# Kernel optimization log

Hardware: AMD Instinct MI355X
Metric: run time of the kernel (lower is better)

Reference implementation:

```python
import jax, jax.numpy as jnp
import numpy as np

DIM = 256
GRID = 5


def setup_inputs() -> dict:
    key = jax.random.key(0)
    kx, kw = jax.random.split(key)
    x = jax.random.normal(kx, (32, 2048, DIM), dtype=jnp.float32)
    scale = 1.0 / (np.sqrt(DIM) * np.sqrt(GRID))
    fourier_weight = jax.random.normal(kw, (2, DIM, DIM, GRID), dtype=jnp.float32) * scale
    bias = jnp.zeros((DIM,), dtype=jnp.float32)
    return {"x": x, "fourier_weight": fourier_weight, "bias": bias}


def reference(x, fourier_weight, bias):
    D = bias.shape[0]
    G = fourier_weight.shape[-1]
    out_shape = x.shape[:-1] + (D,)
    xf = x.reshape(-1, D)                                  # (N, D)
    k = jnp.arange(1, G + 1, dtype=x.dtype)                # (G,)
    arg = xf[:, :, None] * k                               # (N, D, G)
    # y[n,o] = sum_{d,g} cos(k_g x[n,d]) W[0,o,d,g] + sin(k_g x[n,d]) W[1,o,d,g] + b[o]
    y = jnp.einsum('ndg,odg->no', jnp.cos(arg), fourier_weight[0])
    y = y + jnp.einsum('ndg,odg->no', jnp.sin(arg), fourier_weight[1])
    y = y + bias
    return y.reshape(out_shape)
```

## Files before the change

kernel.cpp:

```cpp
#include <hip/hip_runtime.h>
#include <hip/hip_bf16.h>
#include <stdint.h>

#define DIM 256
#define GRID_G 5
#define KTOT (DIM * GRID_G * 2)
#define BM 256
#define BN 256
#define BK 64
#define NTHREADS 512
#define NCHUNK (KTOT / BK)
#define AS_SH (BM * BK)
#define BS_SH (BN * BK)

typedef float f32x4 __attribute__((ext_vector_type(4)));
typedef short bf16x8 __attribute__((ext_vector_type(8)));

static __device__ __forceinline__ uint32_t f2bf_bits(float v) {
    uint32_t u = __float_as_uint(v);
    return (u + 0x7FFFu + ((u >> 16) & 1u)) >> 16;
}

static __device__ __forceinline__ void gload_lds16(const void* g, void* l) {
    __builtin_amdgcn_global_load_lds(
        (const __attribute__((address_space(1))) void*)g,
        (__attribute__((address_space(3))) void*)l, 16, 0, 0);
}

__global__ void wtransform(const float* __restrict__ W, uint16_t* __restrict__ Wb) {
    int idx = blockIdx.x * blockDim.x + threadIdx.x;
    if (idx >= DIM * KTOT) return;
    int o = idx / KTOT;
    int k = idx - o * KTOT;
    int g = k >> 9;
    int r = k & 511;
    int d = r >> 1;
    int s = r & 1;
    float w = W[(((s * DIM + o) * DIM + d) * GRID_G) + g];
    Wb[idx] = (uint16_t)f2bf_bits(w);
}

__global__ __launch_bounds__(NTHREADS, 2)
void fourier_gemm(const float* __restrict__ x, const uint16_t* __restrict__ Wb,
                  const float* __restrict__ bias, float* __restrict__ out) {
    __shared__ __align__(16) short As[2 * AS_SH];
    __shared__ __align__(16) short Bs[2 * BS_SH];

    const int tid  = threadIdx.x;
    const int lane = tid & 63;
    const int wave = tid >> 6;
    const int wrow = wave >> 2;
    const int wcol = wave & 3;
    const int row0 = blockIdx.x * BM;
    const int q16  = (lane >> 4) << 4;

    f32x4 acc[8][4];
#pragma unroll
    for (int m = 0; m < 8; ++m)
#pragma unroll
        for (int n = 0; n < 4; ++n)
            acc[m][n] = (f32x4){0.f, 0.f, 0.f, 0.f};

    const int sd2 = tid & 15;
    const int sn  = tid >> 4;

    float2 xq[8];

#define STAGE_B(cc, buf)                                                      \
    {                                                                         \
        const char* wbb = (const char*)Wb + (size_t)(cc) * 128;               \
        char* dst = (char*)(Bs + (buf) * BS_SH);                              \
        _Pragma("unroll")                                                     \
        for (int i = 0; i < 4; ++i) {                                         \
            int f = tid * 16 + i * 8192;                                      \
            int o = f >> 7;                                                   \
            int col = f & 127;                                                \
            int scol = col ^ ((o & 7) << 4);                                  \
            gload_lds16(wbb + (size_t)o * (KTOT * 2) + scol, dst + f);        \
        }                                                                     \
    }

#define LOAD_X(cc)                                                            \
    {                                                                         \
        int d0 = ((cc) & 7) * 32;                                             \
        _Pragma("unroll")                                                     \
        for (int i = 0; i < 8; ++i) {                                         \
            int n = sn + i * 32;                                              \
            xq[i] = *(const float2*)&x[(size_t)(row0 + n) * DIM + d0 + 2 * sd2]; \
        }                                                                     \
    }

#define TRIG_WRITE(cc, buf)                                                   \
    {                                                                         \
        float kgrev = (float)(((cc) >> 3) + 1) * 0.15915494309189535f;        \
        char* abase = (char*)(As + (buf) * AS_SH);                            \
        _Pragma("unroll")                                                     \
        for (int i = 0; i < 8; ++i) {                                         \
            int n = sn + i * 32;                                              \
            float r0 = xq[i].x * kgrev;                                       \
            float r1 = xq[i].y * kgrev;                                       \
            float s0, c0, s1, c1;                                             \
            asm("v_sin_f32 %0, %1" : "=v"(s0) : "v"(r0));                     \
            asm("v_cos_f32 %0, %1" : "=v"(c0) : "v"(r0));                     \
            asm("v_sin_f32 %0, %1" : "=v"(s1) : "v"(r1));                     \
            asm("v_cos_f32 %0, %1" : "=v"(c1) : "v"(r1));                     \
            uint32_t p0, p1;                                                  \
            asm("v_cvt_pk_bf16_f32 %0, %1, %2" : "=v"(p0) : "v"(c0), "v"(s0));\
            asm("v_cvt_pk_bf16_f32 %0, %1, %2" : "=v"(p1) : "v"(c1), "v"(s1));\
            int boff = (n * 128 + sd2 * 8) ^ ((n & 7) << 4);                  \
            uint64_t pk = ((uint64_t)p1 << 32) | (uint64_t)p0;                \
            *(uint64_t*)(abase + boff) = pk;                                  \
        }                                                                     \
    }

    STAGE_B(0, 0);
    LOAD_X(0);
    TRIG_WRITE(0, 0);
    __syncthreads();

    for (int c = 0; c < NCHUNK; ++c) {
        const int cur = c & 1;
        const int nxt = cur ^ 1;

        if (c + 1 < NCHUNK) {
            STAGE_B(c + 1, nxt);
            LOAD_X(c + 1);
        }

        const char* Ac = (const char*)(As + cur * AS_SH);
        const char* Bc = (const char*)(Bs + cur * BS_SH);

#pragma unroll
        for (int ks = 0; ks < 2; ++ks) {
            bf16x8 af[8], bfr[4];
#pragma unroll
            for (int m = 0; m < 8; ++m) {
                int r = wrow * 128 + m * 16 + (lane & 15);
                int off = (r * 128 + ks * 64 + q16) ^ ((r & 7) << 4);
                af[m] = *(const bf16x8*)(Ac + off);
            }
#pragma unroll
            for (int nf = 0; nf < 4; ++nf) {
                int o = wcol * 64 + nf * 16 + (lane & 15);
                int off = (o * 128 + ks * 64 + q16) ^ ((o & 7) << 4);
                bfr[nf] = *(const bf16x8*)(Bc + off);
            }
#pragma unroll
            for (int m = 0; m < 8; ++m)
#pragma unroll
                for (int nf = 0; nf < 4; ++nf)
                    acc[m][nf] = __builtin_amdgcn_mfma_f32_16x16x32_bf16(
                        af[m], bfr[nf], acc[m][nf], 0, 0, 0);
        }

        if (c + 1 < NCHUNK) {
            TRIG_WRITE(c + 1, nxt);
        }

        __syncthreads();
    }

#pragma unroll
    for (int nf = 0; nf < 4; ++nf) {
        int ocol = wcol * 64 + nf * 16 + (lane & 15);
        float b = bias[ocol];
#pragma unroll
        for (int m = 0; m < 8; ++m) {
            int rbase = row0 + wrow * 128 + m * 16 + ((lane >> 4) << 2);
#pragma unroll
            for (int r = 0; r < 4; ++r) {
                out[(size_t)(rbase + r) * DIM + ocol] = acc[m][nf][r] + b;
            }
        }
    }
}

extern "C" void kernel_launch(void* const* d_in, const int* in_sizes, int n_in,
                              void* d_out, int out_size, void* d_ws, size_t ws_size,
                              hipStream_t stream) {
    const float* x    = (const float*)d_in[0];
    const float* W    = (const float*)d_in[1];
    const float* bias = (const float*)d_in[2];
    float* out        = (float*)d_out;
    uint16_t* Wb      = (uint16_t*)d_ws;

    int rows = in_sizes[0] / DIM;
    int wtot = DIM * KTOT;

    hipLaunchKernelGGL(wtransform, dim3((wtot + 255) / 256), dim3(256), 0, stream, W, Wb);
    hipLaunchKernelGGL(fourier_gemm, dim3(rows / BM), dim3(NTHREADS), 0, stream,
                       x, Wb, bias, out);
}
```

Baseline: 200.5 us.

## Read B fragments directly from global, halve row tile, reorder K loop to reuse x loads

The GEMM kernel stops staging the bf16 weight matrix through LDS and instead has each wave load its B fragments straight from global memory (expected to hit L2). The row tile drops from 256 to 128, LDS use shrinks to the A buffer only, and occupancy is raised to 4 blocks per CU. The K loop is reordered so each slice of x is loaded once and reused across all five frequency multiples, which removes four of every five x reloads. The weight-transform kernel now writes 16-byte vectors per thread. The risk is higher global and L2 traffic for the weights with less latency hiding, since those loads are not prefetched ahead of the MFMAs.

```diff
diff --git a/kernel.cpp b/kernel.cpp
--- a/kernel.cpp
+++ b/kernel.cpp
@@ -4,14 +4,13 @@
 
 #define DIM 256
 #define GRID_G 5
-#define KTOT (DIM * GRID_G * 2)
-#define BM 256
+#define KTOT 2560
+#define BM 128
 #define BN 256
 #define BK 64
 #define NTHREADS 512
 #define NCHUNK (KTOT / BK)
 #define AS_SH (BM * BK)
-#define BS_SH (BN * BK)
 
 typedef float f32x4 __attribute__((ext_vector_type(4)));
 typedef short bf16x8 __attribute__((ext_vector_type(8)));
@@ -21,30 +20,30 @@
     return (u + 0x7FFFu + ((u >> 16) & 1u)) >> 16;
 }
 
-static __device__ __forceinline__ void gload_lds16(const void* g, void* l) {
-    __builtin_amdgcn_global_load_lds(
-        (const __attribute__((address_space(1))) void*)g,
-        (__attribute__((address_space(3))) void*)l, 16, 0, 0);
+__global__ void wtransform(const float* __restrict__ W, uint16_t* __restrict__ Wb) {
+    int t = blockIdx.x * blockDim.x + threadIdx.x;
+    if (t >= DIM * KTOT / 8) return;
+    int o  = t / (KTOT / 8);
+    int k8 = t - o * (KTOT / 8);
+    int k0 = k8 * 8;
+    int g  = k0 >> 9;
+    int r  = k0 & 511;
+    int d0 = r >> 1;
+    union { uint16_t v[8]; uint4 q; } u;
+#pragma unroll
+    for (int j = 0; j < 8; ++j) {
+        int d = d0 + (j >> 1);
+        int s = j & 1;
+        float w = W[(((s * DIM + o) * DIM + d) * GRID_G) + g];
+        u.v[j] = (uint16_t)f2bf_bits(w);
+    }
+    *(uint4*)((char*)Wb + (size_t)t * 16) = u.q;
 }
 
-__global__ void wtransform(const float* __restrict__ W, uint16_t* __restrict__ Wb) {
-    int idx = blockIdx.x * blockDim.x + threadIdx.x;
-    if (idx >= DIM * KTOT) return;
-    int o = idx / KTOT;
-    int k = idx - o * KTOT;
-    int g = k >> 9;
-    int r = k & 511;
-    int d = r >> 1;
-    int s = r & 1;
-    float w = W[(((s * DIM + o) * DIM + d) * GRID_G) + g];
-    Wb[idx] = (uint16_t)f2bf_bits(w);
-}
-
-__global__ __launch_bounds__(NTHREADS, 2)
+__global__ __launch_bounds__(NTHREADS, 4)
 void fourier_gemm(const float* __restrict__ x, const uint16_t* __restrict__ Wb,
                   const float* __restrict__ bias, float* __restrict__ out) {
     __shared__ __align__(16) short As[2 * AS_SH];
-    __shared__ __align__(16) short Bs[2 * BS_SH];
 
     const int tid  = threadIdx.x;
     const int lane = tid & 63;
@@ -54,9 +53,9 @@
     const int row0 = blockIdx.x * BM;
     const int q16  = (lane >> 4) << 4;
 
-    f32x4 acc[8][4];
+    f32x4 acc[4][4];
 #pragma unroll
-    for (int m = 0; m < 8; ++m)
+    for (int m = 0; m < 4; ++m)
 #pragma unroll
         for (int n = 0; n < 4; ++n)
             acc[m][n] = (f32x4){0.f, 0.f, 0.f, 0.f};
@@ -64,38 +63,24 @@
     const int sd2 = tid & 15;
     const int sn  = tid >> 4;
 
-    float2 xq[8];
+    float2 xq[4];
 
-#define STAGE_B(cc, buf)                                                      \
+#define LOAD_X(dr_)                                                           \
     {                                                                         \
-        const char* wbb = (const char*)Wb + (size_t)(cc) * 128;               \
-        char* dst = (char*)(Bs + (buf) * BS_SH);                              \
         _Pragma("unroll")                                                     \
         for (int i = 0; i < 4; ++i) {                                         \
-            int f = tid * 16 + i * 8192;                                      \
-            int o = f >> 7;                                                   \
-            int col = f & 127;                                                \
-            int scol = col ^ ((o & 7) << 4);                                  \
-            gload_lds16(wbb + (size_t)o * (KTOT * 2) + scol, dst + f);        \
+            int n = sn + i * 32;                                              \
+            xq[i] = *(const float2*)&x[(size_t)(row0 + n) * DIM +             \
+                                       (dr_) * 32 + 2 * sd2];                 \
         }                                                                     \
     }
 
-#define LOAD_X(cc)                                                            \
+#define TRIG_WRITE(kg1, buf)                                                  \
     {                                                                         \
-        int d0 = ((cc) & 7) * 32;                                             \
-        _Pragma("unroll")                                                     \
-        for (int i = 0; i < 8; ++i) {                                         \
-            int n = sn + i * 32;                                              \
-            xq[i] = *(const float2*)&x[(size_t)(row0 + n) * DIM + d0 + 2 * sd2]; \
-        }                                                                     \
-    }
-
-#define TRIG_WRITE(cc, buf)                                                   \
-    {                                                                         \
-        float kgrev = (float)(((cc) >> 3) + 1) * 0.15915494309189535f;        \
+        float kgrev = (float)(kg1) * 0.15915494309189535f;                    \
         char* abase = (char*)(As + (buf) * AS_SH);                            \
         _Pragma("unroll")                                                     \
-        for (int i = 0; i < 8; ++i) {                                         \
+        for (int i = 0; i < 4; ++i) {                                         \
             int n = sn + i * 32;                                              \
             float r0 = xq[i].x * kgrev;                                       \
             float r1 = xq[i].y * kgrev;                                       \
@@ -113,51 +98,49 @@
         }                                                                     \
     }
 
-    STAGE_B(0, 0);
     LOAD_X(0);
-    TRIG_WRITE(0, 0);
+    TRIG_WRITE(1, 0);
     __syncthreads();
 
-    for (int c = 0; c < NCHUNK; ++c) {
-        const int cur = c & 1;
-        const int nxt = cur ^ 1;
+    int it = 0;
+    for (int dr = 0; dr < 8; ++dr) {
+#pragma unroll
+        for (int g = 0; g < GRID_G; ++g, ++it) {
+            const int cur = it & 1;
+            const int c   = g * 8 + dr;
+            const char* Ac = (const char*)(As + cur * AS_SH);
 
-        if (c + 1 < NCHUNK) {
-            STAGE_B(c + 1, nxt);
-            LOAD_X(c + 1);
-        }
-
-        const char* Ac = (const char*)(As + cur * AS_SH);
-        const char* Bc = (const char*)(Bs + cur * BS_SH);
+            if (g == GRID_G - 1 && dr < 7) { LOAD_X(dr + 1); }
 
 #pragma unroll
-        for (int ks = 0; ks < 2; ++ks) {
-            bf16x8 af[8], bfr[4];
+            for (int ks = 0; ks < 2; ++ks) {
+                bf16x8 bfr[4], af[4];
 #pragma unroll
-            for (int m = 0; m < 8; ++m) {
-                int r = wrow * 128 + m * 16 + (lane & 15);
-                int off = (r * 128 + ks * 64 + q16) ^ ((r & 7) << 4);
-                af[m] = *(const bf16x8*)(Ac + off);
+                for (int nf = 0; nf < 4; ++nf) {
+                    int o = wcol * 64 + nf * 16 + (lane & 15);
+                    bfr[nf] = *(const bf16x8*)((const char*)Wb +
+                              (size_t)o * (KTOT * 2) + c * 128 + ks * 64 + q16);
+                }
+#pragma unroll
+                for (int m = 0; m < 4; ++m) {
+                    int rr  = wrow * 64 + m * 16 + (lane & 15);
+                    int off = (rr * 128 + ks * 64 + q16) ^ ((rr & 7) << 4);
+                    af[m] = *(const bf16x8*)(Ac + off);
+                }
+#pragma unroll
+                for (int m = 0; m < 4; ++m)
+#pragma unroll
+                    for (int nf = 0; nf < 4; ++nf)
+                        acc[m][nf] = __builtin_amdgcn_mfma_f32_16x16x32_bf16(
+                            af[m], bfr[nf], acc[m][nf], 0, 0, 0);
             }
-#pragma unroll
-            for (int nf = 0; nf < 4; ++nf) {
-                int o = wcol * 64 + nf * 16 + (lane & 15);
-                int off = (o * 128 + ks * 64 + q16) ^ ((o & 7) << 4);
-                bfr[nf] = *(const bf16x8*)(Bc + off);
+
+            if (it < NCHUNK - 1) {
+                int kgn = (g == GRID_G - 1) ? 1 : (g + 2);
+                TRIG_WRITE(kgn, cur ^ 1);
             }
-#pragma unroll
-            for (int m = 0; m < 8; ++m)
-#pragma unroll
-                for (int nf = 0; nf < 4; ++nf)
-                    acc[m][nf] = __builtin_amdgcn_mfma_f32_16x16x32_bf16(
-                        af[m], bfr[nf], acc[m][nf], 0, 0, 0);
+            __syncthreads();
         }
-
-        if (c + 1 < NCHUNK) {
-            TRIG_WRITE(c + 1, nxt);
-        }
-
-        __syncthreads();
     }
 
 #pragma unroll
@@ -165,11 +148,11 @@
         int ocol = wcol * 64 + nf * 16 + (lane & 15);
         float b = bias[ocol];
 #pragma unroll
-        for (int m = 0; m < 8; ++m) {
-            int rbase = row0 + wrow * 128 + m * 16 + ((lane >> 4) << 2);
+        for (int m = 0; m < 4; ++m) {
+            int rbase = row0 + wrow * 64 + m * 16 + ((lane >> 4) << 2);
 #pragma unroll
-            for (int r = 0; r < 4; ++r) {
-                out[(size_t)(rbase + r) * DIM + ocol] = acc[m][nf][r] + b;
+            for (int r2 = 0; r2 < 4; ++r2) {
+                out[(size_t)(rbase + r2) * DIM + ocol] = acc[m][nf][r2] + b;
             }
         }
     }
@@ -185,9 +168,9 @@
     uint16_t* Wb      = (uint16_t*)d_ws;
 
     int rows = in_sizes[0] / DIM;
-    int wtot = DIM * KTOT;
+    int wthreads = DIM * KTOT / 8;
 
-    hipLaunchKernelGGL(wtransform, dim3((wtot + 255) / 256), dim3(256), 0, stream, W, Wb);
+    hipLaunchKernelGGL(wtransform, dim3((wthreads + 255) / 256), dim3(256), 0, stream, W, Wb);
     hipLaunchKernelGGL(fourier_gemm, dim3(rows / BM), dim3(NTHREADS), 0, stream,
                        x, Wb, bias, out);
 }
```

Result: slower. 355.8 us (+77.5%).
